# Performance work log

Measured on AMD Instinct MI355X. Metric: run time of the kernel, lower is better.

Reference implementation:

```python
import jax, jax.numpy as jnp
import numpy as np

# --- architecture constants (match init_kwargs) ---
SLEN = 104
PTILE = 8
STEP = 2
N_BANDS = 2
MAX_DET = 2
N_SRC_PARAMS = 2
ENC_C = 20
ENC_HIDDEN = 256
# dim_out_all = 0.5*D*(D+1)*(4+2*n_source_params) + 1 + D  (probs over n_sources + per-count loc/flux mean+logvar)
DIM_OUT = int(0.5 * MAX_DET * (MAX_DET + 1) * (4 + 2 * N_SRC_PARAMS)) + 1 + MAX_DET  # 27


def _p(key, shape, scale=0.02):
    return scale * jax.random.normal(key, shape, dtype=jnp.float32)


def setup_inputs() -> dict:
    key = jax.random.key(0)
    ks = jax.random.split(key, 14)
    flat_in = ENC_C * PTILE * PTILE  # 20*8*8 = 1280
    return {
        "images": jax.random.normal(ks[0], (32, N_BANDS, SLEN, SLEN), dtype=jnp.float32),
        "conv1_w": _p(ks[1], (ENC_C, N_BANDS, 3, 3)),
        "conv1_b": _p(ks[2], (ENC_C,)),
        "conv2_w": _p(ks[3], (ENC_C, ENC_C, 3, 3)),
        "conv2_b": _p(ks[4], (ENC_C,)),
        "fc1_w": _p(ks[5], (ENC_HIDDEN, flat_in)),
        "fc1_b": _p(ks[6], (ENC_HIDDEN,)),
        "fc2_w": _p(ks[7], (ENC_HIDDEN, ENC_HIDDEN)),
        "fc2_b": _p(ks[8], (ENC_HIDDEN,)),
        "fc3_w": _p(ks[9], (ENC_HIDDEN, ENC_HIDDEN)),
        "fc3_b": _p(ks[10], (ENC_HIDDEN,)),
        "fcf_w": _p(ks[11], (DIM_OUT, ENC_HIDDEN)),
        "fcf_b": _p(ks[12], (DIM_OUT,)),
    }


def _tile_images(images):
    # torch tile_images: (B, C, slen, slen) -> (B * n_ptiles, C, P, P), tiles row-major over (x, y)
    B, C = images.shape[0], images.shape[1]
    patches = jax.lax.conv_general_dilated_patches(
        images, filter_shape=(PTILE, PTILE), window_strides=(STEP, STEP), padding="VALID"
    )  # (B, C*P*P, Hn, Wn) with feature dim ordered (C, P, P)
    Hn, Wn = patches.shape[2], patches.shape[3]
    p = patches.reshape(B, C, PTILE, PTILE, Hn, Wn)
    p = p.transpose(0, 4, 5, 1, 2, 3)  # (B, Hn, Wn, C, P, P)
    return p.reshape(B * Hn * Wn, C, PTILE, PTILE)


def _conv(x, w, b):
    y = jax.lax.conv_general_dilated(
        x, w, window_strides=(1, 1), padding="SAME",
        dimension_numbers=("NCHW", "OIHW", "NCHW"),
    )
    return y + b[None, :, None, None]


def reference(images, conv1_w, conv1_b, conv2_w, conv2_b,
              fc1_w, fc1_b, fc2_w, fc2_b, fc3_w, fc3_b, fcf_w, fcf_b):
    ptiles = _tile_images(images)                       # (B*nT, C, P, P)
    h = jax.nn.relu(_conv(ptiles, conv1_w, conv1_b))    # (B*nT, 20, P, P)
    h = jax.nn.relu(_conv(h, conv2_w, conv2_b))
    h = h.reshape(h.shape[0], -1)                       # Flatten -> (B*nT, 1280)
    h = jax.nn.relu(h @ fc1_w.T + fc1_b)
    h = jax.nn.relu(h @ fc2_w.T + fc2_b)
    h = jax.nn.relu(h @ fc3_w.T + fc3_b)
    return h @ fcf_w.T + fcf_b                          # (B*nT, dim_out_all)
```

## Files before the change

### kernel.cpp

```cpp
#include <hip/hip_runtime.h>
#include <hip/hip_bf16.h>

#define NPATCH 76832
#define NBLK   601
#define K1     1280

typedef __attribute__((ext_vector_type(8))) short  short8;
typedef __attribute__((ext_vector_type(4))) float  floatx4;

__device__ __forceinline__ unsigned short f2b(float f) {
    unsigned int u = __builtin_bit_cast(unsigned int, f);
    u += 0x7FFFu + ((u >> 16) & 1u);
    return (unsigned short)(u >> 16);
}
__device__ __forceinline__ float b2f(unsigned short h) {
    unsigned int u = ((unsigned int)h) << 16;
    return __builtin_bit_cast(float, u);
}
__device__ __forceinline__ unsigned int pk2(float a, float b) {
    __hip_bfloat162 h = __float22bfloat162_rn(make_float2(a, b));
    unsigned int u;
    __builtin_memcpy(&u, &h, 4);
    return u;
}

__device__ __forceinline__ void gload_lds16(const unsigned short* g, unsigned short* l) {
    __builtin_amdgcn_global_load_lds(
        (__attribute__((address_space(1))) void*)g,
        (__attribute__((address_space(3))) void*)l,
        16, 0, 0);
}

__device__ __host__ __forceinline__ int swz8(int row, int i) {
    return (((row & 1) * 4 + i) ^ ((row >> 1) & 7));
}

__global__ void prep(const float* __restrict__ f1w, const float* __restrict__ f2w,
                     const float* __restrict__ f3w, const float* __restrict__ c1w,
                     const float* __restrict__ c2w, const float* __restrict__ ffw,
                     unsigned short* __restrict__ W1, unsigned short* __restrict__ W2,
                     unsigned short* __restrict__ W3, unsigned short* __restrict__ W1T,
                     unsigned short* __restrict__ W2T, unsigned short* __restrict__ WfB) {
    int i = blockIdx.x * 256 + threadIdx.x;
    if (i < 327680) { W1[i] = f2b(f1w[i]); return; }
    i -= 327680;
    if (i < 65536) { W2[i] = f2b(f2w[i]); return; }
    i -= 65536;
    if (i < 65536) { W3[i] = f2b(f3w[i]); return; }
    i -= 65536;
    if (i < 1024) {
        int o = i >> 5, k = i & 31;
        unsigned short v = 0;
        if (o < 20 && k < 18) v = f2b(c1w[o * 18 + k]);
        W1T[(o >> 1) * 64 + swz8(o, k >> 3) * 8 + (k & 7)] = v;
        return;
    }
    i -= 1024;
    if (i < 9216) {
        int tap = i >> 10, rem = i & 1023, o = rem >> 5, c = rem & 31;
        unsigned short v = 0;
        if (o < 20 && c < 20) v = f2b(c2w[o * 180 + c * 9 + tap]);
        W2T[tap * 1024 + (o >> 1) * 64 + swz8(o, c >> 3) * 8 + (c & 7)] = v;
        return;
    }
    i -= 9216;
    if (i < 8192) {
        int o = i >> 8, k = i & 255;
        unsigned short v = (o < 27) ? f2b(ffw[o * 256 + k]) : (unsigned short)0;
        int c = k >> 3, pos = (c & ~7) | ((c & 7) ^ (o & 7));
        WfB[o * 256 + pos * 8 + (k & 7)] = v;
    }
}

__global__ __launch_bounds__(256, 3) void conv_mfma(
    const float* __restrict__ img,
    const unsigned short* __restrict__ W1T, const float* __restrict__ b1,
    const unsigned short* __restrict__ W2T, const float* __restrict__ b2,
    unsigned short* __restrict__ X, int row0)
{
    __shared__ alignas(16) unsigned short s_buf[8 * 2048 + 64];
    __shared__ alignas(16) unsigned short s_w1t[1024];
    __shared__ alignas(16) unsigned short s_w2t[9216];
    __shared__ float s_b1[32], s_b2[32];
    constexpr int ZOFF = 8 * 2048;

    const int tid = threadIdx.x;
    for (int d = tid; d < 512; d += 256)  ((unsigned int*)s_w1t)[d] = ((const unsigned int*)W1T)[d];
    for (int d = tid; d < 4608; d += 256) ((unsigned int*)s_w2t)[d] = ((const unsigned int*)W2T)[d];
    if (tid < 32) {
        ((unsigned int*)&s_buf[ZOFF])[tid] = 0u;
        s_b1[tid] = (tid < 20) ? b1[tid] : 0.f;
        s_b2[tid] = (tid < 20) ? b2[tid] : 0.f;
    }

    const int q = tid >> 5, t = tid & 31;
    const int Pl = blockIdx.x * 8 + q;
    const int Pi = row0 + Pl;
    const bool valid = Pi < NPATCH;
    int b = 0, hi = 0, wi = 0;
    if (valid) { b = Pi / 2401; int rem = Pi - b * 2401; hi = rem / 49; wi = rem - hi * 49; }
    const int py = t >> 2, px0 = (t & 3) * 2;
    const float* ib = img + (long long)b * 21632 + (hi * 2) * 104 + (wi * 2);

    float win[2][3][4];
    #pragma unroll
    for (int c = 0; c < 2; ++c)
        #pragma unroll
        for (int dy = 0; dy < 3; ++dy) {
            int ny = py + dy - 1;
            int nyc = ny < 0 ? 0 : (ny > 7 ? 7 : ny);
            #pragma unroll
            for (int dxw = 0; dxw < 4; ++dxw) {
                int nx = px0 + dxw - 1;
                int nxc = nx < 0 ? 0 : (nx > 7 ? 7 : nx);
                win[c][dy][dxw] = ib[c * 10816 + nyc * 104 + nxc];
            }
        }

    #pragma unroll
    for (int j = 0; j < 2; ++j) {
        const int px = px0 + j, pl = py * 8 + px;
        float val[18];
        #pragma unroll
        for (int c = 0; c < 2; ++c)
            #pragma unroll
            for (int dy = 0; dy < 3; ++dy) {
                int ny = py + dy - 1;
                bool rok = valid && ((unsigned)ny < 8u);
                #pragma unroll
                for (int dx = 0; dx < 3; ++dx) {
                    int nx = px + dx - 1;
                    bool ok = rok && ((unsigned)nx < 8u);
                    val[c * 9 + dy * 3 + dx] = ok ? win[c][dy][dx + j] : 0.f;
                }
            }
        alignas(16) unsigned int au[16];
        #pragma unroll
        for (int i = 0; i < 9; ++i) au[i] = pk2(val[2 * i], val[2 * i + 1]);
        #pragma unroll
        for (int i = 9; i < 16; ++i) au[i] = 0u;
        unsigned short* base = &s_buf[q * 2048 + (pl >> 1) * 64];
        #pragma unroll
        for (int i = 0; i < 4; ++i)
            *(uint4*)&base[swz8(pl, i) * 8] = ((const uint4*)au)[i];
    }
    __syncthreads();

    const int wave = tid >> 6, lane = tid & 63;
    const int l15 = lane & 15, quad = lane >> 4;
    const int p0 = wave * 2;

    int boffB[2];
    #pragma unroll
    for (int i = 0; i < 2; ++i) {
        int oo = i * 16 + l15;
        boffB[i] = (oo >> 1) * 64 + swz8(oo, quad) * 8;
    }

    short8 a1f[2];
    #pragma unroll
    for (int mt = 0; mt < 2; ++mt) a1f[mt] = *(const short8*)&s_w1t[boffB[mt]];

    floatx4 acc1[2][2][4] = {};
    #pragma unroll
    for (int pp = 0; pp < 2; ++pp)
        #pragma unroll
        for (int nt = 0; nt < 4; ++nt) {
            int pix = nt * 16 + l15;
            short8 pf = *(const short8*)&s_buf[(p0 + pp) * 2048 + (pix >> 1) * 64 + swz8(pix, quad) * 8];
            #pragma unroll
            for (int mt = 0; mt < 2; ++mt)
                acc1[pp][mt][nt] = __builtin_amdgcn_mfma_f32_16x16x32_bf16(a1f[mt], pf, acc1[pp][mt][nt], 0, 0, 0);
        }

    float bv1[2][4];
    #pragma unroll
    for (int mt = 0; mt < 2; ++mt)
        #pragma unroll
        for (int r = 0; r < 4; ++r) bv1[mt][r] = s_b1[mt * 16 + quad * 4 + r];

    #pragma unroll
    for (int pp = 0; pp < 2; ++pp)
        #pragma unroll
        for (int mt = 0; mt < 2; ++mt)
            #pragma unroll
            for (int nt = 0; nt < 4; ++nt) {
                floatx4 v = acc1[pp][mt][nt];
                uint2 w;
                w.x = pk2(fmaxf(v[0] + bv1[mt][0], 0.f), fmaxf(v[1] + bv1[mt][1], 0.f));
                w.y = pk2(fmaxf(v[2] + bv1[mt][2], 0.f), fmaxf(v[3] + bv1[mt][3], 0.f));
                int pix = nt * 16 + l15;
                int off = (p0 + pp) * 2048 + (pix >> 1) * 64
                        + swz8(pix, mt * 2 + (quad >> 1)) * 8 + (quad & 1) * 4;
                *(uint2*)&s_buf[off] = w;
            }

    int syv[4], pxv[4];
    #pragma unroll
    for (int mt = 0; mt < 4; ++mt) { int p = mt * 16 + l15; syv[mt] = p >> 3; pxv[mt] = p & 7; }

    floatx4 acc2[2][4][2] = {};
    #pragma unroll 1
    for (int dy = 0; dy < 3; ++dy) {
        int sy[4]; bool okY[4];
        #pragma unroll
        for (int mt = 0; mt < 4; ++mt) {
            sy[mt] = syv[mt] + dy - 1;
            okY[mt] = (unsigned)sy[mt] < 8u;
        }
        #pragma unroll
        for (int dx = 0; dx < 3; ++dx) {
            const int tap = dy * 3 + dx;
            short8 bf0 = *(const short8*)&s_w2t[tap * 1024 + boffB[0]];
            short8 bf1 = *(const short8*)&s_w2t[tap * 1024 + boffB[1]];
            #pragma unroll
            for (int mt = 0; mt < 4; ++mt) {
                int sx = pxv[mt] + dx - 1;
                bool ok = okY[mt] & ((unsigned)sx < 8u);
                int ps = sy[mt] * 8 + sx;
                int offl = (ps >> 1) * 64 + swz8(ps, quad) * 8;
                #pragma unroll
                for (int pp = 0; pp < 2; ++pp) {
                    int off = ok ? ((p0 + pp) * 2048 + offl) : (ZOFF + quad * 8);
                    short8 af = *(const short8*)&s_buf[off];
                    acc2[pp][mt][0] = __builtin_amdgcn_mfma_f32_16x16x32_bf16(af, bf0, acc2[pp][mt][0], 0, 0, 0);
                    acc2[pp][mt][1] = __builtin_amdgcn_mfma_f32_16x16x32_bf16(af, bf1, acc2[pp][mt][1], 0, 0, 0);
                }
            }
        }
    }

    #pragma unroll
    for (int pp = 0; pp < 2; ++pp) {
        unsigned short* xrow = X + (long long)(blockIdx.x * 8 + p0 + pp) * K1;
        #pragma unroll
        for (int nt = 0; nt < 2; ++nt) {
            const int col = nt * 16 + l15;
            if (col < 20) {
                const float bv = s_b2[col];
                #pragma unroll
                for (int mt = 0; mt < 4; ++mt) {
                    floatx4 v = acc2[pp][mt][nt];
                    uint2 w;
                    w.x = pk2(fmaxf(v[0] + bv, 0.f), fmaxf(v[1] + bv, 0.f));
                    w.y = pk2(fmaxf(v[2] + bv, 0.f), fmaxf(v[3] + bv, 0.f));
                    *(uint2*)&xrow[col * 64 + mt * 16 + quad * 4] = w;
                }
            }
        }
    }
}

__global__ __launch_bounds__(256, 2) void fc_all(
    const unsigned short* __restrict__ X,
    const unsigned short* __restrict__ W1, const unsigned short* __restrict__ W2,
    const unsigned short* __restrict__ W3, const unsigned short* __restrict__ WfB,
    const float* __restrict__ b1, const float* __restrict__ b2,
    const float* __restrict__ b3, const float* __restrict__ bf_,
    float* __restrict__ out, int row0)
{
    __shared__ alignas(16) unsigned short s_a[64 * 64];
    __shared__ alignas(16) unsigned short s_b[256 * 64];
    __shared__ alignas(16) unsigned short s_h[64 * 256];

    const int tid = threadIdx.x;
    const int m0 = blockIdx.x * 64;
    const int wave = tid >> 6, lane = tid & 63;
    const int l15 = lane & 15, quad = lane >> 4;
    const int lrow = lane >> 3, lchunk = lane & 7;

    floatx4 acc[4][4];

    #pragma unroll
    for (int mt = 0; mt < 4; ++mt)
        #pragma unroll
        for (int nt = 0; nt < 4; ++nt) acc[mt][nt] = floatx4{0.f, 0.f, 0.f, 0.f};

    #pragma unroll 1
    for (int kt = 0; kt < 1280; kt += 64) {
        #pragma unroll
        for (int i = 0; i < 2; ++i) {
            int br = wave * 16 + i * 8, r = br + lrow;
            gload_lds16(X + (long long)(m0 + r) * 1280 + kt + (lchunk ^ (r & 7)) * 8, &s_a[br * 64]);
        }
        #pragma unroll
        for (int i = 0; i < 8; ++i) {
            int br = wave * 64 + i * 8, r = br + lrow;
            gload_lds16(W1 + (long long)r * 1280 + kt + (lchunk ^ (r & 7)) * 8, &s_b[br * 64]);
        }
        __syncthreads();
        #pragma unroll
        for (int kh = 0; kh < 2; ++kh) {
            short8 af[4], bf[4];
            #pragma unroll
            for (int mt = 0; mt < 4; ++mt) {
                int r = wave * 64 + mt * 16 + l15;
                af[mt] = *(const short8*)&s_b[r * 64 + (((kh * 4 + quad) ^ (r & 7)) * 8)];
            }
            #pragma unroll
            for (int nt = 0; nt < 4; ++nt) {
                int r = nt * 16 + l15;
                bf[nt] = *(const short8*)&s_a[r * 64 + (((kh * 4 + quad) ^ (r & 7)) * 8)];
            }
            #pragma unroll
            for (int mt = 0; mt < 4; ++mt)
                #pragma unroll
                for (int nt = 0; nt < 4; ++nt)
                    acc[mt][nt] = __builtin_amdgcn_mfma_f32_16x16x32_bf16(af[mt], bf[nt], acc[mt][nt], 0, 0, 0);
        }
        __syncthreads();
    }
    {
        #pragma unroll
        for (int mt = 0; mt < 4; ++mt) {
            int obase = wave * 64 + mt * 16 + quad * 4;
            float v0 = b1[obase], v1 = b1[obase + 1], v2 = b1[obase + 2], v3 = b1[obase + 3];
            int clow = mt * 2 + (quad >> 1), sub = (quad & 1) * 4;
            #pragma unroll
            for (int nt = 0; nt < 4; ++nt) {
                int row = nt * 16 + l15;
                int pos = wave * 8 + (clow ^ (row & 7));
                floatx4 v = acc[mt][nt];
                uint2 w;
                w.x = pk2(fmaxf(v[0] + v0, 0.f), fmaxf(v[1] + v1, 0.f));
                w.y = pk2(fmaxf(v[2] + v2, 0.f), fmaxf(v[3] + v3, 0.f));
                *(uint2*)&s_h[row * 256 + pos * 8 + sub] = w;
            }
        }
    }
    __syncthreads();

    #pragma unroll 1
    for (int layer = 0; layer < 2; ++layer) {
        const unsigned short* Wp = (layer == 0) ? W2 : W3;
        const float* bp = (layer == 0) ? b2 : b3;

        #pragma unroll
        for (int mt = 0; mt < 4; ++mt)
            #pragma unroll
            for (int nt = 0; nt < 4; ++nt) acc[mt][nt] = floatx4{0.f, 0.f, 0.f, 0.f};

        #pragma unroll 1
        for (int kt2 = 0; kt2 < 4; ++kt2) {
            #pragma unroll
            for (int i = 0; i < 8; ++i) {
                int br = wave * 64 + i * 8, r = br + lrow;
                gload_lds16(Wp + (long long)r * 256 + kt2 * 64 + (lchunk ^ (r & 7)) * 8, &s_b[br * 64]);
            }
            __syncthreads();
            #pragma unroll
            for (int kh = 0; kh < 2; ++kh) {
                short8 af[4], bf[4];
                #pragma unroll
                for (int mt = 0; mt < 4; ++mt) {
                    int r = wave * 64 + mt * 16 + l15;
                    af[mt] = *(const short8*)&s_b[r * 64 + (((kh * 4 + quad) ^ (r & 7)) * 8)];
                }
                #pragma unroll
                for (int nt = 0; nt < 4; ++nt) {
                    int row = nt * 16 + l15;
                    int pos = kt2 * 8 + ((kh * 4 + quad) ^ (row & 7));
                    bf[nt] = *(const short8*)&s_h[row * 256 + pos * 8];
                }
                #pragma unroll
                for (int mt = 0; mt < 4; ++mt)
                    #pragma unroll
                    for (int nt = 0; nt < 4; ++nt)
                        acc[mt][nt] = __builtin_amdgcn_mfma_f32_16x16x32_bf16(af[mt], bf[nt], acc[mt][nt], 0, 0, 0);
            }
            __syncthreads();
        }
        #pragma unroll
        for (int mt = 0; mt < 4; ++mt) {
            int obase = wave * 64 + mt * 16 + quad * 4;
            float v0 = bp[obase], v1 = bp[obase + 1], v2 = bp[obase + 2], v3 = bp[obase + 3];
            int clow = mt * 2 + (quad >> 1), sub = (quad & 1) * 4;
            #pragma unroll
            for (int nt = 0; nt < 4; ++nt) {
                int row = nt * 16 + l15;
                int pos = wave * 8 + (clow ^ (row & 7));
                floatx4 v = acc[mt][nt];
                uint2 w;
                w.x = pk2(fmaxf(v[0] + v0, 0.f), fmaxf(v[1] + v1, 0.f));
                w.y = pk2(fmaxf(v[2] + v2, 0.f), fmaxf(v[3] + v3, 0.f));
                *(uint2*)&s_h[row * 256 + pos * 8 + sub] = w;
            }
        }
        __syncthreads();
    }

    #pragma unroll
    for (int i = 0; i < 4; ++i) {
        int cbase = i * 256 + wave * 64;
        gload_lds16(WfB + (long long)(cbase + lane) * 8, &s_b[cbase * 8]);
    }
    __syncthreads();

    floatx4 accf[2] = {};
    const int myrow = wave * 16 + l15;
    #pragma unroll
    for (int w8 = 0; w8 < 8; ++w8) {
        int chi = w8 >> 1, clo = (w8 & 1) * 4 + quad;
        short8 bfr = *(const short8*)&s_h[myrow * 256 + (chi * 8 + (clo ^ (myrow & 7))) * 8];
        #pragma unroll
        for (int mt = 0; mt < 2; ++mt) {
            int o = mt * 16 + l15;
            short8 afr = *(const short8*)&s_b[o * 256 + (chi * 8 + (clo ^ (o & 7))) * 8];
            accf[mt] = __builtin_amdgcn_mfma_f32_16x16x32_bf16(afr, bfr, accf[mt], 0, 0, 0);
        }
    }
    const int grow = row0 + m0 + myrow;
    if (grow < NPATCH) {
        #pragma unroll
        for (int mt = 0; mt < 2; ++mt) {
            #pragma unroll
            for (int r = 0; r < 4; ++r) {
                int o = mt * 16 + quad * 4 + r;
                if (o < 27)
                    out[(long long)grow * 27 + o] = accf[mt][r] + bf_[o];
            }
        }
    }
}

extern "C" void kernel_launch(void* const* d_in, const int* in_sizes, int n_in,
                              void* d_out, int out_size, void* d_ws, size_t ws_size,
                              hipStream_t stream) {
    const float* images = (const float*)d_in[0];
    const float* c1w = (const float*)d_in[1];
    const float* c1b = (const float*)d_in[2];
    const float* c2w = (const float*)d_in[3];
    const float* c2b = (const float*)d_in[4];
    const float* f1w = (const float*)d_in[5];
    const float* f1b = (const float*)d_in[6];
    const float* f2w = (const float*)d_in[7];
    const float* f2b_ = (const float*)d_in[8];
    const float* f3w = (const float*)d_in[9];
    const float* f3b = (const float*)d_in[10];
    const float* ffw = (const float*)d_in[11];
    const float* ffb = (const float*)d_in[12];

    const long long W1_E = 327680, W2_E = 65536, W3_E = 65536;
    const long long W1T_E = 1024, W2T_E = 9216, WF_E = 8192;
    const long long WB = (W1_E + W2_E + W3_E + W1T_E + W2T_E + WF_E) * 2;
    char* ws = (char*)d_ws;
    unsigned short* W1  = (unsigned short*)ws;
    unsigned short* W2  = W1 + W1_E;
    unsigned short* W3  = W2 + W2_E;
    unsigned short* W1T = W3 + W3_E;
    unsigned short* W2T = W1T + W1T_E;
    unsigned short* WfB = W2T + W2T_E;
    unsigned short* X   = (unsigned short*)(ws + WB);

    long long avail = (long long)ws_size - WB - 256;
    int nb_max = (int)(avail / 327680LL);
    if (nb_max < 1) nb_max = 1;
    if (nb_max > NBLK) nb_max = NBLK;
    int nchunks = (NBLK + nb_max - 1) / nb_max;
    int nb_even = (NBLK + nchunks - 1) / nchunks;

    prep<<<1864, 256, 0, stream>>>(f1w, f2w, f3w, c1w, c2w, ffw, W1, W2, W3, W1T, W2T, WfB);

    for (int b0 = 0; b0 < NBLK; b0 += nb_even) {
        int nb = NBLK - b0; if (nb > nb_even) nb = nb_even;
        int row0 = b0 * 128;
        int rows = nb * 128;

        conv_mfma<<<rows / 8, 256, 0, stream>>>(images, W1T, c1b, W2T, c2b, X, row0);
        fc_all<<<rows / 64, 256, 0, stream>>>(X, W1, W2, W3, WfB,
                                              f1b, f2b_, f3b, ffb, (float*)d_out, row0);
    }
}
```

Baseline: 332.8 us.

## Load FC weights and activations directly from global memory, dropping LDS staging

The fc_all kernel no longer stages X and weight tiles through shared memory with global_load_lds and barriers. Each lane now reads its MFMA fragments straight from global memory (relying on L1/L2 caching), and the final-layer weights are stored unswizzled and read directly. Shared memory drops to the hidden activation buffer only, and launch bounds rise to 3 blocks per CU to raise occupancy. The trade-off is more redundant global and L2 traffic, since each weight fragment is now fetched separately by every wave that uses it instead of once per block.

```diff
diff --git a/kernel.cpp b/kernel.cpp
--- a/kernel.cpp
+++ b/kernel.cpp
@@ -12,23 +12,12 @@
     unsigned int u = __builtin_bit_cast(unsigned int, f);
     u += 0x7FFFu + ((u >> 16) & 1u);
     return (unsigned short)(u >> 16);
-}
-__device__ __forceinline__ float b2f(unsigned short h) {
-    unsigned int u = ((unsigned int)h) << 16;
-    return __builtin_bit_cast(float, u);
 }
 __device__ __forceinline__ unsigned int pk2(float a, float b) {
     __hip_bfloat162 h = __float22bfloat162_rn(make_float2(a, b));
     unsigned int u;
     __builtin_memcpy(&u, &h, 4);
     return u;
-}
-
-__device__ __forceinline__ void gload_lds16(const unsigned short* g, unsigned short* l) {
-    __builtin_amdgcn_global_load_lds(
-        (__attribute__((address_space(1))) void*)g,
-        (__attribute__((address_space(3))) void*)l,
-        16, 0, 0);
 }
 
 __device__ __host__ __forceinline__ int swz8(int row, int i) {
@@ -66,9 +55,7 @@
     i -= 9216;
     if (i < 8192) {
         int o = i >> 8, k = i & 255;
-        unsigned short v = (o < 27) ? f2b(ffw[o * 256 + k]) : (unsigned short)0;
-        int c = k >> 3, pos = (c & ~7) | ((c & 7) ^ (o & 7));
-        WfB[o * 256 + pos * 8 + (k & 7)] = v;
+        WfB[i] = (o < 27) ? f2b(ffw[o * 256 + k]) : (unsigned short)0;
     }
 }
 
@@ -251,7 +238,7 @@
     }
 }
 
-__global__ __launch_bounds__(256, 2) void fc_all(
+__global__ __launch_bounds__(256, 3) void fc_all(
     const unsigned short* __restrict__ X,
     const unsigned short* __restrict__ W1, const unsigned short* __restrict__ W2,
     const unsigned short* __restrict__ W3, const unsigned short* __restrict__ WfB,
@@ -259,15 +246,12 @@
     const float* __restrict__ b3, const float* __restrict__ bf_,
     float* __restrict__ out, int row0)
 {
-    __shared__ alignas(16) unsigned short s_a[64 * 64];
-    __shared__ alignas(16) unsigned short s_b[256 * 64];
     __shared__ alignas(16) unsigned short s_h[64 * 256];
 
     const int tid = threadIdx.x;
     const int m0 = blockIdx.x * 64;
     const int wave = tid >> 6, lane = tid & 63;
     const int l15 = lane & 15, quad = lane >> 4;
-    const int lrow = lane >> 3, lchunk = lane & 7;
 
     floatx4 acc[4][4];
 
@@ -276,45 +260,85 @@
         #pragma unroll
         for (int nt = 0; nt < 4; ++nt) acc[mt][nt] = floatx4{0.f, 0.f, 0.f, 0.f};
 
-    #pragma unroll 1
-    for (int kt = 0; kt < 1280; kt += 64) {
-        #pragma unroll
-        for (int i = 0; i < 2; ++i) {
-            int br = wave * 16 + i * 8, r = br + lrow;
-            gload_lds16(X + (long long)(m0 + r) * 1280 + kt + (lchunk ^ (r & 7)) * 8, &s_a[br * 64]);
-        }
-        #pragma unroll
-        for (int i = 0; i < 8; ++i) {
-            int br = wave * 64 + i * 8, r = br + lrow;
-            gload_lds16(W1 + (long long)r * 1280 + kt + (lchunk ^ (r & 7)) * 8, &s_b[br * 64]);
-        }
-        __syncthreads();
-        #pragma unroll
-        for (int kh = 0; kh < 2; ++kh) {
+    {
+        const unsigned short* wb[4];
+        const unsigned short* xb[4];
+        #pragma unroll
+        for (int mt = 0; mt < 4; ++mt)
+            wb[mt] = W1 + (long long)(wave * 64 + mt * 16 + l15) * 1280 + quad * 8;
+        #pragma unroll
+        for (int nt = 0; nt < 4; ++nt)
+            xb[nt] = X + (long long)(m0 + nt * 16 + l15) * 1280 + quad * 8;
+
+        #pragma unroll 2
+        for (int k = 0; k < 1280; k += 32) {
             short8 af[4], bf[4];
             #pragma unroll
-            for (int mt = 0; mt < 4; ++mt) {
-                int r = wave * 64 + mt * 16 + l15;
-                af[mt] = *(const short8*)&s_b[r * 64 + (((kh * 4 + quad) ^ (r & 7)) * 8)];
-            }
-            #pragma unroll
-            for (int nt = 0; nt < 4; ++nt) {
-                int r = nt * 16 + l15;
-                bf[nt] = *(const short8*)&s_a[r * 64 + (((kh * 4 + quad) ^ (r & 7)) * 8)];
-            }
+            for (int mt = 0; mt < 4; ++mt) af[mt] = *(const short8*)(wb[mt] + k);
+            #pragma unroll
+            for (int nt = 0; nt < 4; ++nt) bf[nt] = *(const short8*)(xb[nt] + k);
             #pragma unroll
             for (int mt = 0; mt < 4; ++mt)
                 #pragma unroll
                 for (int nt = 0; nt < 4; ++nt)
                     acc[mt][nt] = __builtin_amdgcn_mfma_f32_16x16x32_bf16(af[mt], bf[nt], acc[mt][nt], 0, 0, 0);
         }
+    }
+    #pragma unroll
+    for (int mt = 0; mt < 4; ++mt) {
+        int obase = wave * 64 + mt * 16 + quad * 4;
+        float v0 = b1[obase], v1 = b1[obase + 1], v2 = b1[obase + 2], v3 = b1[obase + 3];
+        int clow = mt * 2 + (quad >> 1), sub = (quad & 1) * 4;
+        #pragma unroll
+        for (int nt = 0; nt < 4; ++nt) {
+            int row = nt * 16 + l15;
+            int pos = wave * 8 + (clow ^ (row & 7));
+            floatx4 v = acc[mt][nt];
+            uint2 w;
+            w.x = pk2(fmaxf(v[0] + v0, 0.f), fmaxf(v[1] + v1, 0.f));
+            w.y = pk2(fmaxf(v[2] + v2, 0.f), fmaxf(v[3] + v3, 0.f));
+            *(uint2*)&s_h[row * 256 + pos * 8 + sub] = w;
+        }
+    }
+    __syncthreads();
+
+    #pragma unroll 1
+    for (int layer = 0; layer < 2; ++layer) {
+        const unsigned short* Wp = (layer == 0) ? W2 : W3;
+        const float* bp = (layer == 0) ? b2 : b3;
+
+        #pragma unroll
+        for (int mt = 0; mt < 4; ++mt)
+            #pragma unroll
+            for (int nt = 0; nt < 4; ++nt) acc[mt][nt] = floatx4{0.f, 0.f, 0.f, 0.f};
+
+        const unsigned short* wb[4];
+        #pragma unroll
+        for (int mt = 0; mt < 4; ++mt)
+            wb[mt] = Wp + (long long)(wave * 64 + mt * 16 + l15) * 256 + quad * 8;
+
+        #pragma unroll
+        for (int it = 0; it < 8; ++it) {
+            short8 af[4], bf[4];
+            #pragma unroll
+            for (int mt = 0; mt < 4; ++mt) af[mt] = *(const short8*)(wb[mt] + it * 32);
+            int chi = it >> 1, clo4 = (it & 1) * 4 + quad;
+            #pragma unroll
+            for (int nt = 0; nt < 4; ++nt) {
+                int row = nt * 16 + l15;
+                bf[nt] = *(const short8*)&s_h[row * 256 + (chi * 8 + (clo4 ^ (row & 7))) * 8];
+            }
+            #pragma unroll
+            for (int mt = 0; mt < 4; ++mt)
+                #pragma unroll
+                for (int nt = 0; nt < 4; ++nt)
+                    acc[mt][nt] = __builtin_amdgcn_mfma_f32_16x16x32_bf16(af[mt], bf[nt], acc[mt][nt], 0, 0, 0);
+        }
         __syncthreads();
-    }
-    {
         #pragma unroll
         for (int mt = 0; mt < 4; ++mt) {
             int obase = wave * 64 + mt * 16 + quad * 4;
-            float v0 = b1[obase], v1 = b1[obase + 1], v2 = b1[obase + 2], v3 = b1[obase + 3];
+            float v0 = bp[obase], v1 = bp[obase + 1], v2 = bp[obase + 2], v3 = bp[obase + 3];
             int clow = mt * 2 + (quad >> 1), sub = (quad & 1) * 4;
             #pragma unroll
             for (int nt = 0; nt < 4; ++nt) {
@@ -327,74 +351,8 @@
                 *(uint2*)&s_h[row * 256 + pos * 8 + sub] = w;
             }
         }
-    }
-    __syncthreads();
-
-    #pragma unroll 1
-    for (int layer = 0; layer < 2; ++layer) {
-        const unsigned short* Wp = (layer == 0) ? W2 : W3;
-        const float* bp = (layer == 0) ? b2 : b3;
-
-        #pragma unroll
-        for (int mt = 0; mt < 4; ++mt)
-            #pragma unroll
-            for (int nt = 0; nt < 4; ++nt) acc[mt][nt] = floatx4{0.f, 0.f, 0.f, 0.f};
-
-        #pragma unroll 1
-        for (int kt2 = 0; kt2 < 4; ++kt2) {
-            #pragma unroll
-            for (int i = 0; i < 8; ++i) {
-                int br = wave * 64 + i * 8, r = br + lrow;
-                gload_lds16(Wp + (long long)r * 256 + kt2 * 64 + (lchunk ^ (r & 7)) * 8, &s_b[br * 64]);
-            }
-            __syncthreads();
-            #pragma unroll
-            for (int kh = 0; kh < 2; ++kh) {
-                short8 af[4], bf[4];
-                #pragma unroll
-                for (int mt = 0; mt < 4; ++mt) {
-                    int r = wave * 64 + mt * 16 + l15;
-                    af[mt] = *(const short8*)&s_b[r * 64 + (((kh * 4 + quad) ^ (r & 7)) * 8)];
-                }
-                #pragma unroll
-                for (int nt = 0; nt < 4; ++nt) {
-                    int row = nt * 16 + l15;
-                    int pos = kt2 * 8 + ((kh * 4 + quad) ^ (row & 7));
-                    bf[nt] = *(const short8*)&s_h[row * 256 + pos * 8];
-                }
-                #pragma unroll
-                for (int mt = 0; mt < 4; ++mt)
-                    #pragma unroll
-                    for (int nt = 0; nt < 4; ++nt)
-                        acc[mt][nt] = __builtin_amdgcn_mfma_f32_16x16x32_bf16(af[mt], bf[nt], acc[mt][nt], 0, 0, 0);
-            }
-            __syncthreads();
-        }
-        #pragma unroll
-        for (int mt = 0; mt < 4; ++mt) {
-            int obase = wave * 64 + mt * 16 + quad * 4;
-            float v0 = bp[obase], v1 = bp[obase + 1], v2 = bp[obase + 2], v3 = bp[obase + 3];
-            int clow = mt * 2 + (quad >> 1), sub = (quad & 1) * 4;
-            #pragma unroll
-            for (int nt = 0; nt < 4; ++nt) {
-                int row = nt * 16 + l15;
-                int pos = wave * 8 + (clow ^ (row & 7));
-                floatx4 v = acc[mt][nt];
-                uint2 w;
-                w.x = pk2(fmaxf(v[0] + v0, 0.f), fmaxf(v[1] + v1, 0.f));
-                w.y = pk2(fmaxf(v[2] + v2, 0.f), fmaxf(v[3] + v3, 0.f));
-                *(uint2*)&s_h[row * 256 + pos * 8 + sub] = w;
-            }
-        }
         __syncthreads();
     }
-
-    #pragma unroll
-    for (int i = 0; i < 4; ++i) {
-        int cbase = i * 256 + wave * 64;
-        gload_lds16(WfB + (long long)(cbase + lane) * 8, &s_b[cbase * 8]);
-    }
-    __syncthreads();
 
     floatx4 accf[2] = {};
     const int myrow = wave * 16 + l15;
@@ -405,7 +363,7 @@
         #pragma unroll
         for (int mt = 0; mt < 2; ++mt) {
             int o = mt * 16 + l15;
-            short8 afr = *(const short8*)&s_b[o * 256 + (chi * 8 + (clo ^ (o & 7))) * 8];
+            short8 afr = *(const short8*)(WfB + o * 256 + w8 * 32 + quad * 8);
             accf[mt] = __builtin_amdgcn_mfma_f32_16x16x32_bf16(afr, bfr, accf[mt], 0, 0, 0);
         }
     }
```

Measured after the change: 487.5 us. +46.5%, slower.
